# Kernel optimization log

Hardware: AMD Instinct MI355X
Metric: run time of the kernel (lower is better)

## Reference

```python
import jax, jax.numpy as jnp
import numpy as np

T, B, H, V = 1024, 64, 256, 32000


def setup_inputs() -> dict:
    key = jax.random.key(0)
    ks = jax.random.split(key, 12)
    inputSequence = jax.random.randint(ks[0], (T, B), 0, V)
    lengths = jax.random.randint(ks[1], (B,), 1, T + 1)
    lengths = jnp.sort(lengths)[::-1]          # pack_padded_sequence needs descending
    lengths = lengths.at[0].set(T)             # max length == padded length
    s = 1.0 / np.sqrt(H)
    def w(k, shape):
        return jax.random.uniform(k, shape, jnp.float32, -s, s)
    return {
        "inputSequence": inputSequence,
        "inputLengths": lengths,
        "embedding": jax.random.normal(ks[2], (V, H), jnp.float32),
        "W_ih_f": w(ks[3], (3 * H, H)), "W_hh_f": w(ks[4], (3 * H, H)),
        "b_ih_f": w(ks[5], (3 * H,)),   "b_hh_f": w(ks[6], (3 * H,)),
        "W_ih_b": w(ks[7], (3 * H, H)), "W_hh_b": w(ks[8], (3 * H, H)),
        "b_ih_b": w(ks[9], (3 * H,)),   "b_hh_b": w(ks[10], (3 * H,)),
    }


def _gru_dir(emb, mask, Wih, Whh, bih, bhh, reverse):
    # emb: (T,B,H), mask: (T,B). PyTorch GRU cell math.
    Tn, Bn, Hn = emb.shape
    xg = emb @ Wih.T + bih                      # (T,B,3H) input-side gates precomputed
    def step(h, inp):
        xg_t, m = inp
        hg = h @ Whh.T + bhh                    # (B,3H)
        r = jax.nn.sigmoid(xg_t[:, :Hn] + hg[:, :Hn])
        z = jax.nn.sigmoid(xg_t[:, Hn:2 * Hn] + hg[:, Hn:2 * Hn])
        n = jnp.tanh(xg_t[:, 2 * Hn:] + r * hg[:, 2 * Hn:])
        h_new = (1.0 - z) * n + z * h
        m_ = m[:, None]
        h_next = jnp.where(m_, h_new, h)        # packed seq: frozen past length
        y = jnp.where(m_, h_new, 0.0)           # pad_packed zeros padded steps
        return h_next, y
    h0 = jnp.zeros((Bn, Hn), emb.dtype)
    hT, ys = jax.lax.scan(step, h0, (xg, mask), reverse=reverse)
    return ys, hT


def reference(inputSequence, inputLengths, embedding,
              W_ih_f, W_hh_f, b_ih_f, b_hh_f,
              W_ih_b, W_hh_b, b_ih_b, b_hh_b):
    Tn, Bn = inputSequence.shape
    emb = embedding[inputSequence]                              # (T,B,H)
    mask = jnp.arange(Tn)[:, None] < inputLengths[None, :]      # (T,B)
    yf, hf = _gru_dir(emb, mask, W_ih_f, W_hh_f, b_ih_f, b_hh_f, False)
    yb, hb = _gru_dir(emb, mask, W_ih_b, W_hh_b, b_ih_b, b_hh_b, True)
    outputs = yf + yb                                           # sum fwd/bwd halves
    hidden = jnp.stack([hf, hb], axis=0)                        # (2, B, H)
    return outputs, hidden
```

## Files before the change

kernel.cpp:

```cpp
#include <hip/hip_runtime.h>


typedef __attribute__((ext_vector_type(8))) short short8;
typedef __attribute__((ext_vector_type(4))) float floatx4;

__device__ __forceinline__ float rcp_(float x) { return __builtin_amdgcn_rcpf(x); }
__device__ __forceinline__ float sigmoid_(float x) { return rcp_(1.0f + __expf(-x)); }
__device__ __forceinline__ float tanh_(float x)    { return 1.0f - 2.0f * rcp_(1.0f + __expf(2.0f * x)); }
__device__ __forceinline__ unsigned short f2bf(float f) {
  unsigned int u = __float_as_uint(f);
  return (unsigned short)((u + 0x7fffu + ((u >> 16) & 1u)) >> 16);
}


__global__ __launch_bounds__(256) void prep_embB(
    const float* __restrict__ emb, unsigned short* __restrict__ embB) {
  int i4 = blockIdx.x * 256 + threadIdx.x;
  float4 v = ((const float4*)emb)[i4];
  ushort4 o;
  o.x = f2bf(v.x); o.y = f2bf(v.y); o.z = f2bf(v.z); o.w = f2bf(v.w);
  ((ushort4*)embB)[i4] = o;
}

__global__ __launch_bounds__(256) void prep_packB(
    const float* __restrict__ wf, const float* __restrict__ wb,
    unsigned short* __restrict__ oB) {
  int idx = blockIdx.x * 256 + threadIdx.x;
  int d = idx >= 196608;
  int o = idx - d * 196608;
  int jj   = o & 7;
  int lane = (o >> 3) & 63;
  int rest = o >> 9;
  int nt   = rest % 48;
  int kc   = rest / 48;
  int n = nt * 16 + (lane & 15);
  int k = kc * 32 + ((lane >> 4) << 3) + jj;
  const float* w = d ? wb : wf;
  oB[idx] = f2bf(w[n * 256 + k]);
}

__global__ __launch_bounds__(256) void prep_packA(
    const float* __restrict__ wf, const float* __restrict__ wb,
    unsigned short* __restrict__ oA) {
  int idx = blockIdx.x * 256 + threadIdx.x;
  int d = idx >= 196608;
  int o = idx - d * 196608;
  int jj   = o & 7;
  int lane = (o >> 3) & 63;
  int kc   = (o >> 9) & 7;
  int tl   = o >> 12;
  int row  = tl * 16 + (lane & 15);
  int k    = kc * 32 + ((lane >> 4) << 3) + jj;
  const float* w = d ? wb : wf;
  oA[idx] = f2bf(w[row * 256 + k]);
}

__global__ __launch_bounds__(512, 2) void fused_step(
    const int* __restrict__ seq, const int* __restrict__ lens,
    const unsigned short* __restrict__ embB,
    const unsigned short* __restrict__ pWihB,
    const unsigned short* __restrict__ pA,
    const float* __restrict__ bih_f, const float* __restrict__ bih_b,
    const float* __restrict__ bhh_f, const float* __restrict__ bhh_b,
    float* __restrict__ out, float* __restrict__ hcar,
    const float* __restrict__ xs_f, const float* __restrict__ xs_b,
    float* __restrict__ xw_f, float* __restrict__ xw_b,
    int nscan, int s_base_f, int s_base_b, int Tc, int is_last, int do_add,
    int xg_on, int x_base_f, int x_base_b) {
  __shared__ __align__(16) unsigned char smem[49152];
  const int bid = (int)blockIdx.x;
  const int tid = threadIdx.x;
  const int lane = tid & 63;

  if (bid < nscan) {
    __builtin_amdgcn_s_setprio(1);
    const int wv  = tid >> 6;
    const int qp  = bid >> 1;
    const int dir = bid & 1;
    const int b0  = qp * 2;

    const float* xg  = dir ? xs_b : xs_f;
    const float* bhh = dir ? bhh_b : bhh_f;
    const int len0 = lens[b0], len1 = lens[b0 + 1];
    const int lenmax = len0 > len1 ? len0 : len1;
    const int base = dir ? s_base_b : s_base_f;

    short8 af[6][8];
    {
      const short8* pA8 = (const short8*)(pA + (size_t)dir * 196608);
#pragma unroll
      for (int i = 0; i < 6; ++i)
#pragma unroll
        for (int kc = 0; kc < 8; ++kc)
          af[i][kc] = pA8[(((wv * 6 + i) * 8 + kc) << 6) + lane];
    }

    unsigned short* hbf = (unsigned short*)smem;
    float*          res = (float*)(smem + 1280);

    const int b  = tid >> 8;
    const int j  = tid & 255;
    const int bb = b0 + b;
    const int blen = b ? len1 : len0;
    float hreg = hcar[dir * 16384 + bb * 256 + j];
    const float bhn = bhh[512 + j];
    hbf[b * 288 + j] = f2bf(hreg);
    __syncthreads();

    int s_lo, s_hi;
    if (dir == 0) { s_lo = 0; int e = lenmax - base; s_hi = e < 0 ? 0 : (e > Tc ? Tc : e); }
    else { int sk = base + Tc - lenmax; s_lo = sk < 0 ? 0 : (sk > Tc ? Tc : sk); s_hi = Tc; }

    const int nB = lane & 15, qq = lane >> 4;
    const bool bld = nB < 2;
    const unsigned short* hsrc = &hbf[nB * 288 + qq * 8];

    float xr = 0.f, xz = 0.f, xn = 0.f, oprev = 0.f;
    if (s_lo < s_hi) {
      const int t0  = dir ? (base + (Tc - 1 - s_lo)) : (base + s_lo);
      const float* xrow = xg + ((size_t)(t0 - base) * 64 + bb) * 768 + j;
      xr = xrow[0]; xz = xrow[256]; xn = xrow[512];
      if (do_add) oprev = out[((size_t)t0 * 64 + bb) * 256 + j];
    }

    for (int s = s_lo; s < s_hi; ++s) {
      const int t  = dir ? (base + (Tc - 1 - s)) : (base + s);
      const bool act = t < blen;

      const int sn = (s + 1 < s_hi) ? s + 1 : s;
      const int tn = dir ? (base + (Tc - 1 - sn)) : (base + sn);
      float xr2, xz2, xn2, oprev2 = 0.f;
      {
        const float* xrow = xg + ((size_t)(tn - base) * 64 + bb) * 768 + j;
        xr2 = xrow[0]; xz2 = xrow[256]; xn2 = xrow[512];
        if (do_add) oprev2 = out[((size_t)tn * 64 + bb) * 256 + j];
      }

      floatx4 acc[6];
#pragma unroll
      for (int i = 0; i < 6; ++i) acc[i] = (floatx4){0.f, 0.f, 0.f, 0.f};

#pragma unroll
      for (int kc = 0; kc < 8; ++kc) {
        short8 bfr = {0, 0, 0, 0, 0, 0, 0, 0};
        if (bld) bfr = *(const short8*)(hsrc + kc * 32);
#pragma unroll
        for (int i = 0; i < 6; ++i)
          acc[i] = __builtin_amdgcn_mfma_f32_16x16x32_bf16(af[i][kc], bfr, acc[i], 0, 0, 0);
      }

      if (bld) {
#pragma unroll
        for (int i = 0; i < 6; ++i) {
          int r0 = (wv * 6 + i) * 16 + qq * 4;
          *(floatx4*)&res[nB * 784 + r0] = acc[i];
        }
      }
      __syncthreads();

      float ar = res[b * 784 + j];
      float az = res[b * 784 + 256 + j];
      float an = res[b * 784 + 512 + j];
      float r  = sigmoid_(xr + ar);
      float z  = sigmoid_(xz + az);
      float nn = tanh_(xn + r * (an + bhn));
      float hn = (1.0f - z) * nn + z * hreg;
      if (act) {
        hreg = hn;
        hbf[b * 288 + j] = f2bf(hn);
        out[((size_t)t * 64 + bb) * 256 + j] = do_add ? (oprev + hn) : hn;
      }
      __syncthreads();

      xr = xr2; xz = xz2; xn = xn2; oprev = oprev2;
    }

    hcar[dir * 16384 + bb * 256 + j] = hreg;
    if (is_last)
      out[(size_t)1024 * 64 * 256 + (size_t)dir * 16384 + bb * 256 + j] = hreg;

  } else if (xg_on) {
    const int idx  = bid - nscan;
    const int sx   = idx >> 1;
    const int dir  = idx & 1;
    const int w    = tid >> 6;
    const int mt   = w & 3;
    const int h2   = w >> 2;
    const int t    = (dir ? x_base_b : x_base_f) + sx;
    const int c    = lane & 15, qq = lane >> 4;

    const float* bih = dir ? bih_b : bih_f;
    const float* bhh = dir ? bhh_b : bhh_f;
    float* xgo = (dir ? xw_b : xw_f) + (size_t)sx * 64 * 768;

    const int tk = seq[t * 64 + mt * 16 + c];
    const unsigned short* aptr = embB + (size_t)tk * 256 + qq * 8;
    short8 afr[8];
#pragma unroll
    for (int kc = 0; kc < 8; ++kc) afr[kc] = *(const short8*)(aptr + kc * 32);

    float4* Bs4 = (float4*)smem;

    floatx4 acc[24];
#pragma unroll
    for (int q = 0; q < 24; ++q) acc[q] = (floatx4){0.f, 0.f, 0.f, 0.f};

    for (int kc = 0; kc < 8; ++kc) {
      __syncthreads();
      const float4* src = (const float4*)(pWihB + (size_t)dir * 196608 + kc * 24576);
#pragma unroll
      for (int i = 0; i < 6; ++i) Bs4[tid + i * 512] = src[tid + i * 512];
      __syncthreads();
      const short8* bsv = (const short8*)Bs4;
      short8 af = afr[kc];
#pragma unroll
      for (int q = 0; q < 24; ++q) {
        int nt = h2 * 24 + q;
        acc[q] = __builtin_amdgcn_mfma_f32_16x16x32_bf16(af, bsv[nt * 64 + lane], acc[q], 0, 0, 0);
      }
    }

#pragma unroll
    for (int q = 0; q < 24; ++q) {
      int n = (h2 * 24 + q) * 16 + c;
      float bv = bih[n] + (n < 512 ? bhh[n] : 0.0f);
#pragma unroll
      for (int r = 0; r < 4; ++r)
        xgo[(size_t)(mt * 16 + qq * 4 + r) * 768 + n] = acc[q][r] + bv;
    }
  }
}

extern "C" void kernel_launch(void* const* d_in, const int* in_sizes, int n_in,
                              void* d_out, int out_size, void* d_ws, size_t ws_size,
                              hipStream_t stream) {
  const int*   seq   = (const int*)d_in[0];
  const int*   lens  = (const int*)d_in[1];
  const float* emb   = (const float*)d_in[2];
  const float* Wih_f = (const float*)d_in[3];
  const float* Whh_f = (const float*)d_in[4];
  const float* bih_f = (const float*)d_in[5];
  const float* bhh_f = (const float*)d_in[6];
  const float* Wih_b = (const float*)d_in[7];
  const float* Whh_b = (const float*)d_in[8];
  const float* bih_b = (const float*)d_in[9];
  const float* bhh_b = (const float*)d_in[10];
  float* out = (float*)d_out;
  float* ws  = (float*)d_ws;

  float*          hcar   = ws;
  unsigned short* pA     = (unsigned short*)(ws + 32768);
  unsigned short* pWihB  = (unsigned short*)(ws + 229376);
  unsigned short* embB   = (unsigned short*)(ws + 425984);
  float*          xgbase = ws + 4521984;

  int Tc = 8;
  const int cands[7] = {512, 256, 128, 64, 32, 16, 8};
  for (int i = 0; i < 7; ++i) {
    size_t need = (4521984ull + 4ull * (size_t)cands[i] * 49152ull) * 4ull;
    if (need <= ws_size) { Tc = cands[i]; break; }
  }
  const int C = 1024 / Tc;
  float* xb[2][2];
  for (int p = 0; p < 2; ++p)
    for (int d = 0; d < 2; ++d)
      xb[p][d] = xgbase + ((size_t)(p * 2 + d)) * Tc * 49152;

  hipMemsetAsync(d_out, 0, (size_t)1024 * 64 * 256 * 4, stream);
  hipMemsetAsync(hcar, 0, 32768ull * 4ull, stream);
  prep_embB<<<dim3(8000), dim3(256), 0, stream>>>(emb, embB);
  prep_packB<<<dim3(1536), dim3(256), 0, stream>>>(Wih_f, Wih_b, pWihB);
  prep_packA<<<dim3(1536), dim3(256), 0, stream>>>(Whh_f, Whh_b, pA);

  fused_step<<<dim3(2 * Tc), dim3(512), 0, stream>>>(
      seq, lens, embB, pWihB, pA, bih_f, bih_b, bhh_f, bhh_b, out, hcar,
      xb[0][0], xb[0][1], xb[0][0], xb[0][1],
      0, 0, 0, Tc, 0, 0, 1, 0, (C - 1) * Tc);

  for (int c = 0; c < C; ++c) {
    int xgon = (c + 1 < C) ? 1 : 0;
    int nblk = 64 + (xgon ? 2 * Tc : 0);
    fused_step<<<dim3(nblk), dim3(512), 0, stream>>>(
        seq, lens, embB, pWihB, pA, bih_f, bih_b, bhh_f, bhh_b, out, hcar,
        xb[c & 1][0], xb[c & 1][1], xb[(c + 1) & 1][0], xb[(c + 1) & 1][1],
        64, c * Tc, (C - 1 - c) * Tc, Tc,
        (c == C - 1) ? 1 : 0, (2 * c >= C) ? 1 : 0,
        xgon, (c + 1) * Tc, (C - 2 - c) * Tc);
  }
}
```

Baseline: 1.688 ms.

## Use non-uniform chunk schedule and split MFMA accumulators into even/odd chains

The host chunking of the time dimension changes from uniform Tc chunks to a symmetric plan of 64,224,224,224,224,64 steps when the workspace allows. Short first and last chunks shrink the unoverlapped input-gate precompute prologue and the tail chunk. Inside the recurrent step, all eight h fragments are loaded up front and the MFMA chain is split into two independent accumulator sets, which shortens the dependency chain but doubles accumulator registers. The symmetric plan is needed because forward and backward directions index chunks from opposite ends.

```diff
diff --git a/kernel.cpp b/kernel.cpp
--- a/kernel.cpp
+++ b/kernel.cpp
@@ -136,24 +136,35 @@
         if (do_add) oprev2 = out[((size_t)tn * 64 + bb) * 256 + j];
       }
 
-      floatx4 acc[6];
-#pragma unroll
-      for (int i = 0; i < 6; ++i) acc[i] = (floatx4){0.f, 0.f, 0.f, 0.f};
-
-#pragma unroll
-      for (int kc = 0; kc < 8; ++kc) {
-        short8 bfr = {0, 0, 0, 0, 0, 0, 0, 0};
-        if (bld) bfr = *(const short8*)(hsrc + kc * 32);
+      short8 bfr[8];
+#pragma unroll
+      for (int kc = 0; kc < 8; ++kc) bfr[kc] = (short8){0, 0, 0, 0, 0, 0, 0, 0};
+      if (bld) {
+#pragma unroll
+        for (int kc = 0; kc < 8; ++kc) bfr[kc] = *(const short8*)(hsrc + kc * 32);
+      }
+
+      floatx4 accE[6], accO[6];
+#pragma unroll
+      for (int i = 0; i < 6; ++i) {
+        accE[i] = (floatx4){0.f, 0.f, 0.f, 0.f};
+        accO[i] = (floatx4){0.f, 0.f, 0.f, 0.f};
+      }
+#pragma unroll
+      for (int kc = 0; kc < 8; kc += 2) {
 #pragma unroll
         for (int i = 0; i < 6; ++i)
-          acc[i] = __builtin_amdgcn_mfma_f32_16x16x32_bf16(af[i][kc], bfr, acc[i], 0, 0, 0);
+          accE[i] = __builtin_amdgcn_mfma_f32_16x16x32_bf16(af[i][kc], bfr[kc], accE[i], 0, 0, 0);
+#pragma unroll
+        for (int i = 0; i < 6; ++i)
+          accO[i] = __builtin_amdgcn_mfma_f32_16x16x32_bf16(af[i][kc + 1], bfr[kc + 1], accO[i], 0, 0, 0);
       }
 
       if (bld) {
 #pragma unroll
         for (int i = 0; i < 6; ++i) {
           int r0 = (wv * 6 + i) * 16 + qq * 4;
-          *(floatx4*)&res[nB * 784 + r0] = acc[i];
+          *(floatx4*)&res[nB * 784 + r0] = accE[i] + accO[i];
         }
       }
       __syncthreads();
@@ -254,17 +265,31 @@
   unsigned short* embB   = (unsigned short*)(ws + 425984);
   float*          xgbase = ws + 4521984;
 
-  int Tc = 8;
-  const int cands[7] = {512, 256, 128, 64, 32, 16, 8};
-  for (int i = 0; i < 7; ++i) {
-    size_t need = (4521984ull + 4ull * (size_t)cands[i] * 49152ull) * 4ull;
-    if (need <= ws_size) { Tc = cands[i]; break; }
+  int S[128], off[128], C = 0, Smax = 0;
+  {
+    size_t needA = (4521984ull + 4ull * 224ull * 49152ull) * 4ull;
+    if (needA <= ws_size) {
+      const int plan[6] = {64, 224, 224, 224, 224, 64};
+      C = 6;
+      for (int i = 0; i < C; ++i) S[i] = plan[i];
+    } else {
+      const int cands[7] = {512, 256, 128, 64, 32, 16, 8};
+      int Tc = 8;
+      for (int i = 0; i < 7; ++i) {
+        size_t need = (4521984ull + 4ull * (size_t)cands[i] * 49152ull) * 4ull;
+        if (need <= ws_size) { Tc = cands[i]; break; }
+      }
+      C = 1024 / Tc;
+      for (int i = 0; i < C; ++i) S[i] = Tc;
+    }
+    int o = 0;
+    for (int i = 0; i < C; ++i) { off[i] = o; o += S[i]; if (S[i] > Smax) Smax = S[i]; }
   }
-  const int C = 1024 / Tc;
+
   float* xb[2][2];
   for (int p = 0; p < 2; ++p)
     for (int d = 0; d < 2; ++d)
-      xb[p][d] = xgbase + ((size_t)(p * 2 + d)) * Tc * 49152;
+      xb[p][d] = xgbase + ((size_t)(p * 2 + d)) * Smax * 49152;
 
   hipMemsetAsync(d_out, 0, (size_t)1024 * 64 * 256 * 4, stream);
   hipMemsetAsync(hcar, 0, 32768ull * 4ull, stream);
@@ -272,19 +297,20 @@
   prep_packB<<<dim3(1536), dim3(256), 0, stream>>>(Wih_f, Wih_b, pWihB);
   prep_packA<<<dim3(1536), dim3(256), 0, stream>>>(Whh_f, Whh_b, pA);
 
-  fused_step<<<dim3(2 * Tc), dim3(512), 0, stream>>>(
+  fused_step<<<dim3(2 * S[0]), dim3(512), 0, stream>>>(
       seq, lens, embB, pWihB, pA, bih_f, bih_b, bhh_f, bhh_b, out, hcar,
       xb[0][0], xb[0][1], xb[0][0], xb[0][1],
-      0, 0, 0, Tc, 0, 0, 1, 0, (C - 1) * Tc);
+      0, 0, 0, S[0], 0, 0,
+      1, off[0], off[C - 1]);
 
   for (int c = 0; c < C; ++c) {
     int xgon = (c + 1 < C) ? 1 : 0;
-    int nblk = 64 + (xgon ? 2 * Tc : 0);
+    int nblk = 64 + (xgon ? 2 * S[c + 1] : 0);
     fused_step<<<dim3(nblk), dim3(512), 0, stream>>>(
         seq, lens, embB, pWihB, pA, bih_f, bih_b, bhh_f, bhh_b, out, hcar,
         xb[c & 1][0], xb[c & 1][1], xb[(c + 1) & 1][0], xb[(c + 1) & 1][1],
-        64, c * Tc, (C - 1 - c) * Tc, Tc,
+        64, off[c], off[C - 1 - c], S[c],
         (c == C - 1) ? 1 : 0, (2 * c >= C) ? 1 : 0,
-        xgon, (c + 1) * Tc, (C - 2 - c) * Tc);
+        xgon, xgon ? off[c + 1] : 0, xgon ? off[C - 2 - c] : 0);
   }
 }
```

Result: slower. 3.280 ms (+94.3%).
